# Kernel optimization log

Hardware: AMD Instinct MI355X
Metric: run time of the kernel (lower is better)

The kernel has to match this reference:

```python
import jax, jax.numpy as jnp
import numpy as np

C = 256; G = 16; GC = C // G; K = 3; P = K * K
N = 4; H = 64; W = 64
PAD = 1; OFFSET_SCALE = 1.0; LN_EPS = 1e-5


def setup_inputs() -> dict:
    key = jax.random.key(0)
    ks = jax.random.split(key, 8)
    s = 0.02
    return {
        "x": jax.random.normal(ks[0], (N, C, H, W), jnp.float32),
        "dw_w": jax.random.normal(ks[1], (C, 1, K, K), jnp.float32) * s,
        "dw_b": jnp.zeros((C,), jnp.float32),
        "ln_g": jnp.ones((C,), jnp.float32),
        "ln_b": jnp.zeros((C,), jnp.float32),
        "off_w": jax.random.normal(ks[2], (C, G * P * 2), jnp.float32) * s,
        "off_b": jnp.zeros((G * P * 2,), jnp.float32),
        "mask_w": jax.random.normal(ks[3], (C, G * P), jnp.float32) * s,
        "mask_b": jnp.zeros((G * P,), jnp.float32),
        "inp_w": jax.random.normal(ks[4], (C, C), jnp.float32) * s,
        "inp_b": jnp.zeros((C,), jnp.float32),
        "out_w": jax.random.normal(ks[5], (C, C), jnp.float32) * s,
        "out_b": jnp.zeros((C,), jnp.float32),
    }


def _dcnv3_nchw(x, dw_w, dw_b, ln_g, ln_b, off_w, off_b, mask_w, mask_b,
                inp_w, inp_b, out_w, out_b):
    # NCHW -> NHWC (wrapper permute)
    xn = jnp.transpose(x, (0, 2, 3, 1))                      # (N,H,W,C)
    x_proj = xn @ inp_w + inp_b                              # input_proj

    # offset/mask branch: depthwise conv (NCHW) -> LayerNorm (channels-last) -> GELU
    x1 = jax.lax.conv_general_dilated(
        x, dw_w, window_strides=(1, 1), padding=((PAD, PAD), (PAD, PAD)),
        dimension_numbers=("NCHW", "OIHW", "NCHW"), feature_group_count=C)
    x1 = jnp.transpose(x1, (0, 2, 3, 1)) + dw_b
    mu = x1.mean(-1, keepdims=True)
    var = ((x1 - mu) ** 2).mean(-1, keepdims=True)
    x1 = (x1 - mu) * jax.lax.rsqrt(var + LN_EPS) * ln_g + ln_b
    x1 = jax.nn.gelu(x1, approximate=False)

    offset = (x1 @ off_w + off_b).reshape(N, H, W, G, P, 2)  # (x,y) pairs
    mask = jax.nn.softmax((x1 @ mask_w + mask_b).reshape(N, H, W, G, P), axis=-1)

    # pad sampled feature map with zeros (F.pad before sampling)
    xp = jnp.pad(x_proj, ((0, 0), (PAD, PAD), (PAD, PAD), (0, 0)))
    Hin, Win = H + 2 * PAD, W + 2 * PAD
    xg = xp.reshape(N, Hin, Win, G, GC)

    # reference points, normalized by padded size
    ref_y = (jnp.arange(H, dtype=jnp.float32) + PAD + 0.5) / Hin
    ref_x = (jnp.arange(W, dtype=jnp.float32) + PAD + 0.5) / Win
    ref = jnp.stack([jnp.broadcast_to(ref_x[None, :], (H, W)),
                     jnp.broadcast_to(ref_y[:, None], (H, W))], -1)  # (H,W,2)

    # dilation grid: x varies in the outer loop (torch meshgrid 'ij')
    d = jnp.arange(K, dtype=jnp.float32) - (K - 1) // 2     # [-1,0,1]
    gx = jnp.repeat(d, K) / Win
    gy = jnp.tile(d, K) / Hin
    grid = jnp.stack([gx, gy], -1)                           # (P,2)

    norm = jnp.array([Win, Hin], jnp.float32)
    loc = (ref[None, :, :, None, None, :] + grid * OFFSET_SCALE
           + offset * OFFSET_SCALE / norm)                   # (N,H,W,G,P,2)

    # grid_sample bilinear, align_corners=False, zero padding
    px = loc[..., 0] * Win - 0.5
    py = loc[..., 1] * Hin - 0.5
    x0 = jnp.floor(px); y0 = jnp.floor(py)
    wx = px - x0; wy = py - y0
    x0i = x0.astype(jnp.int32); y0i = y0.astype(jnp.int32)

    n_idx = jnp.arange(N)[:, None, None, None, None]
    g_idx = jnp.arange(G)[None, None, None, :, None]

    def corner(iy, ix, w):
        valid = (iy >= 0) & (iy < Hin) & (ix >= 0) & (ix < Win)
        v = xg[n_idx, jnp.clip(iy, 0, Hin - 1), jnp.clip(ix, 0, Win - 1), g_idx]
        wgt = jnp.where(valid, w, 0.0) * mask                # fold mask into weights
        return jnp.einsum("nhwgp,nhwgpc->nhwgc", wgt, v)

    out = (corner(y0i, x0i, (1 - wy) * (1 - wx))
           + corner(y0i, x0i + 1, (1 - wy) * wx)
           + corner(y0i + 1, x0i, wy * (1 - wx))
           + corner(y0i + 1, x0i + 1, wy * wx))               # (N,H,W,G,GC)

    out = out.reshape(N, H, W, C) @ out_w + out_b            # output_proj
    return jnp.transpose(out, (0, 3, 1, 2))                  # NHWC -> NCHW


def reference(x, dw_w, dw_b, ln_g, ln_b, off_w, off_b, mask_w, mask_b,
              inp_w, inp_b, out_w, out_b):
    return _dcnv3_nchw(x, dw_w, dw_b, ln_g, ln_b, off_w, off_b,
                       mask_w, mask_b, inp_w, inp_b, out_w, out_b)
```

## Files before the change

### kernel.cpp

```cpp
#include <hip/hip_runtime.h>
#include <hip/hip_bf16.h>
#include <math.h>


using bf16x8 = __attribute__((ext_vector_type(8))) short;
using f32x4  = __attribute__((ext_vector_type(4))) float;

#define GLOBAL_AS __attribute__((address_space(1)))
#define LDS_AS    __attribute__((address_space(3)))

static __device__ inline void g2lds16(const void* g, void* l) {
  __builtin_amdgcn_global_load_lds((const GLOBAL_AS int*)g, (LDS_AS int*)l, 16, 0, 0);
}
static __device__ inline unsigned short f2bf(float v) {
  __hip_bfloat16 b = __float2bfloat16(v);
  return *reinterpret_cast<unsigned short*>(&b);
}
static __device__ inline float us2f(unsigned short u) {
  union { unsigned u; float f; } c; c.u = ((unsigned)u) << 16; return c.f;
}

__global__ __launch_bounds__(256) void prep_xt_k(
    const float* __restrict__ x,
    const float* __restrict__ inp_w, const float* __restrict__ off_w,
    const float* __restrict__ off_b, const float* __restrict__ mask_w,
    const float* __restrict__ mask_b, const float* __restrict__ out_w,
    __hip_bfloat16* __restrict__ BtI, __hip_bfloat16* __restrict__ BtOM,
    __hip_bfloat16* __restrict__ BtO, float* __restrict__ bOM,
    __hip_bfloat16* __restrict__ xT)
{
  __shared__ float tile[32][65];
  const int b = blockIdx.x, t = threadIdx.x;
  if (b < 1024) {
    if (b < 256) {
      int n = b;
      BtI[n * 256 + t] = __float2bfloat16(inp_w[t * 256 + n]);
    } else if (b < 768) {
      int n = b - 256;
      float v = 0.f;
      if (n < 288) v = off_w[t * 288 + n];
      else if (n < 432) v = mask_w[t * 144 + (n - 288)];
      BtOM[n * 256 + t] = __float2bfloat16(v);
      if (b == 256) {
        for (int idx = t; idx < 512; idx += 256) {
          float bv = (idx < 288) ? off_b[idx] : ((idx < 432) ? mask_b[idx - 288] : 0.f);
          bOM[idx] = bv;
        }
      }
    } else {
      int n = b - 768;
      BtO[n * 256 + t] = __float2bfloat16(out_w[t * 256 + n]);
    }
    return;
  }
  const int i = b - 1024;
  const int hw0 = (i & 63) * 64, c0 = ((i >> 6) & 7) * 32, n4 = i >> 9;
  #pragma unroll
  for (int r = 0; r < 8; ++r) {
    int idx = t + r * 256;
    int cl = idx >> 6, wl = idx & 63;
    tile[cl][wl] = x[(size_t)n4 * 1048576 + (size_t)(c0 + cl) * 4096 + hw0 + wl];
  }
  __syncthreads();
  #pragma unroll
  for (int r = 0; r < 2; ++r) {
    int idx = t + r * 256;
    int pixl = idx >> 3, cq = idx & 7;
    unsigned short b0 = f2bf(tile[cq * 4 + 0][pixl]);
    unsigned short b1 = f2bf(tile[cq * 4 + 1][pixl]);
    unsigned short b2 = f2bf(tile[cq * 4 + 2][pixl]);
    unsigned short b3 = f2bf(tile[cq * 4 + 3][pixl]);
    uint2 u;
    u.x = (unsigned)b0 | ((unsigned)b1 << 16);
    u.y = (unsigned)b2 | ((unsigned)b3 << 16);
    *(uint2*)&xT[((size_t)n4 * 4096 + hw0 + pixl) * 256 + c0 + cq * 4] = u;
  }
}

struct G64 {
  f32x4 acc[2][2];
  int lane, quad, lr, wm, wn;
};

static __device__ inline void g64_loop(
    G64& g, const __hip_bfloat16* __restrict__ A,
    const __hip_bfloat16* __restrict__ Bt, size_t m0, int n0,
    short* As, short* Bs, int t)
{
  #pragma unroll
  for (int i = 0; i < 2; ++i)
    #pragma unroll
    for (int j = 0; j < 2; ++j)
      g.acc[i][j] = (f32x4){0.f, 0.f, 0.f, 0.f};
  const int row = t >> 2, kq = t & 3;
  for (int kt = 0; kt < 256; kt += 32) {
    g2lds16(A + (m0 + row) * 256 + kt + kq * 8, (char*)As + t * 16);
    g2lds16(Bt + (size_t)(n0 + row) * 256 + kt + kq * 8, (char*)Bs + t * 16);
    __syncthreads();
    bf16x8 bfv[2];
    #pragma unroll
    for (int ni = 0; ni < 2; ++ni)
      bfv[ni] = *(const bf16x8*)&Bs[(g.wn * 32 + ni * 16 + g.lr) * 32 + g.quad * 8];
    #pragma unroll
    for (int mi = 0; mi < 2; ++mi) {
      bf16x8 af = *(const bf16x8*)&As[(g.wm * 32 + mi * 16 + g.lr) * 32 + g.quad * 8];
      #pragma unroll
      for (int ni = 0; ni < 2; ++ni)
        g.acc[mi][ni] = __builtin_amdgcn_mfma_f32_16x16x32_bf16(af, bfv[ni], g.acc[mi][ni], 0, 0, 0);
    }
    __syncthreads();
  }
}

__global__ __launch_bounds__(1024) void stage2_gi_k(
    const __hip_bfloat16* __restrict__ xT,
    const float* __restrict__ dw_w, const float* __restrict__ dw_b,
    const float* __restrict__ ln_g, const float* __restrict__ ln_b,
    const __hip_bfloat16* __restrict__ BtOM, const float* __restrict__ bOM,
    __hip_bfloat16* __restrict__ om,
    const __hip_bfloat16* __restrict__ BtI, const float* __restrict__ inp_b,
    __hip_bfloat16* __restrict__ xpu)
{
  __shared__ __align__(16) char smem[62464];
  const int bid = blockIdx.x;

  if (bid >= 256) {
    const int sb = threadIdx.x >> 8;
    const int t = threadIdx.x & 255;
    const int tile = (bid - 256) * 4 + sb;
    const int n0 = (tile & 3) * 64;
    const size_t m0 = (size_t)(tile >> 2) * 64;
    short* As = (short*)(smem + sb * 8192);
    short* Bs = (short*)(smem + sb * 8192 + 4096);

    G64 g;
    g.lane = t & 63; g.quad = g.lane >> 4; g.lr = g.lane & 15;
    int wave = t >> 6;
    g.wm = wave >> 1; g.wn = wave & 1;
    g64_loop(g, xT, BtI, m0, n0, As, Bs, t);

    #pragma unroll
    for (int mi = 0; mi < 2; ++mi) {
      #pragma unroll
      for (int ni = 0; ni < 2; ++ni) {
        int col = n0 + g.wn * 32 + ni * 16 + g.lr;
        float bv = inp_b[col];
        #pragma unroll
        for (int reg = 0; reg < 4; ++reg) {
          size_t m = m0 + g.wm * 32 + mi * 16 + g.quad * 4 + reg;
          xpu[m * 256 + col] = __float2bfloat16(g.acc[mi][ni][reg] + bv);
        }
      }
    }
    return;
  }

  unsigned short* x1t = (unsigned short*)smem;
  unsigned short* xs  = (unsigned short*)(smem + 33792);
  float* wgt  = (float*)(smem + 33792 + 15360);
  float* psq  = (float*)(smem + 33792 + 15360 + 1152);
  float* murs = (float*)(smem + 33792 + 15360 + 1152 + 8192);
  short* Bs   = (short*)(smem + 33792);

  const int blk = ((bid & 7) << 5) | (bid >> 3);
  const int n4 = blk >> 6, h = blk & 63;
  const int t = threadIdx.x;
  const int w = t & 63, q = t >> 6;

  float s1 = 0.f, s2 = 0.f;
  for (int chunk = 0; chunk < 8; ++chunk) {
    const int ch0 = chunk * 32;
    if (t < 768) {
      int r = t >> 8, i = t & 255;
      int px = i >> 2, cq = i & 3;
      int hh = h + r - 1;
      uint4 v = {0, 0, 0, 0};
      if ((unsigned)hh < 64u)
        v = *(const uint4*)(xT + ((size_t)n4 * 4096 + (size_t)hh * 64 + px) * 256 + ch0 + cq * 8);
      *(uint4*)&xs[(r * 64 + px) * 40 + cq * 8] = v;
    }
    if (t < 288) {
      int p = t >> 5, lc = t & 31;
      wgt[p * 32 + lc] = dw_w[(ch0 + lc) * 9 + p];
    }
    __syncthreads();
    {
      int c = ch0 + 2 * q;
      float a0 = dw_b[c], a1 = dw_b[c + 1];
      #pragma unroll
      for (int p = 0; p < 9; ++p) {
        int dh = p / 3, dwd = p % 3 - 1;
        int ww = w + dwd;
        if ((unsigned)ww < 64u) {
          unsigned xv = *(const unsigned*)&xs[(dh * 64 + ww) * 40 + 2 * q];
          float wa = wgt[p * 32 + 2 * q], wb = wgt[p * 32 + 2 * q + 1];
          a0 = fmaf(us2f((unsigned short)(xv & 0xffff)), wa, a0);
          a1 = fmaf(us2f((unsigned short)(xv >> 16)), wb, a1);
        }
      }
      s1 += a0 + a1;
      s2 = fmaf(a0, a0, fmaf(a1, a1, s2));
      unsigned pk = (unsigned)f2bf(a0) | ((unsigned)f2bf(a1) << 16);
      *(unsigned*)&x1t[w * 264 + c] = pk;
    }
    __syncthreads();
  }

  psq[q * 64 + w] = s1;
  psq[1024 + q * 64 + w] = s2;
  __syncthreads();
  if (t < 64) {
    float a = 0.f, b = 0.f;
    #pragma unroll
    for (int j = 0; j < 16; ++j) { a += psq[j * 64 + t]; b += psq[1024 + j * 64 + t]; }
    float mu = a * (1.f / 256.f);
    murs[t] = mu;
    murs[64 + t] = rsqrtf(b * (1.f / 256.f) - mu * mu + 1e-5f);
  }
  __syncthreads();
  {
    float mu = murs[w], rs = murs[64 + w];
    #pragma unroll
    for (int chunk = 0; chunk < 8; ++chunk) {
      int c = chunk * 32 + 2 * q;
      unsigned pk = *(const unsigned*)&x1t[w * 264 + c];
      float v0 = us2f((unsigned short)(pk & 0xffff));
      float v1 = us2f((unsigned short)(pk >> 16));
      float y0 = fmaf((v0 - mu) * rs, ln_g[c], ln_b[c]);
      float y1 = fmaf((v1 - mu) * rs, ln_g[c + 1], ln_b[c + 1]);
      float g0 = 0.5f * y0 * (1.f + erff(y0 * 0.70710678f));
      float g1 = 0.5f * y1 * (1.f + erff(y1 * 0.70710678f));
      *(unsigned*)&x1t[w * 264 + c] = (unsigned)f2bf(g0) | ((unsigned)f2bf(g1) << 16);
    }
  }
  __syncthreads();

  const int wave = t >> 6, lane = t & 63;
  const int quad = lane >> 4, lr = lane & 15;
  const int wm = wave >> 2, wn = wave & 3;
  f32x4 acc[7];
  #pragma unroll
  for (int i = 0; i < 7; ++i) acc[i] = (f32x4){0.f, 0.f, 0.f, 0.f};

  for (int kt = 0; kt < 256; kt += 32) {
    __syncthreads();
    {
      int col = t >> 2, kq = t & 3;
      g2lds16(BtOM + (size_t)col * 256 + kt + kq * 8, (char*)Bs + t * 16);
      int j = t + 1024;
      if (j < 1792) {
        col = j >> 2; kq = j & 3;
        g2lds16(BtOM + (size_t)col * 256 + kt + kq * 8, (char*)Bs + j * 16);
      }
    }
    __syncthreads();
    bf16x8 af = *(const bf16x8*)&x1t[(wm * 16 + lr) * 264 + kt + quad * 8];
    #pragma unroll
    for (int ni = 0; ni < 7; ++ni) {
      bf16x8 bf = *(const bf16x8*)&Bs[(wn * 112 + ni * 16 + lr) * 32 + quad * 8];
      acc[ni] = __builtin_amdgcn_mfma_f32_16x16x32_bf16(af, bf, acc[ni], 0, 0, 0);
    }
  }

  const size_t pix0 = (size_t)n4 * 4096 + (size_t)h * 64;
  #pragma unroll
  for (int ni = 0; ni < 7; ++ni) {
    int col = wn * 112 + ni * 16 + lr;
    if (col < 432) {
      float bv = bOM[col];
      #pragma unroll
      for (int reg = 0; reg < 4; ++reg) {
        int m = wm * 16 + quad * 4 + reg;
        om[(pix0 + m) * 448 + col] = __float2bfloat16(acc[ni][reg] + bv);
      }
    }
  }
}

__global__ __launch_bounds__(1024) void fused_so_k(
    const __hip_bfloat16* __restrict__ xpu, const __hip_bfloat16* __restrict__ om,
    const __hip_bfloat16* __restrict__ BtO, const float* __restrict__ out_b,
    float* __restrict__ out)
{
  __shared__ __align__(16) char smem[50176];
  unsigned short* st = (unsigned short*)smem;
  short* Bs = (short*)(smem + 33792);

  const int bid = blockIdx.x;
  const int swz = ((bid & 7) << 5) | (bid >> 3);
  const int pix0 = swz << 6;
  const int t = threadIdx.x;

  {
    const int pl = t >> 4, g = t & 15;
    const int pix = pix0 + pl;
    const int n4s = pix >> 12;
    const int hw = pix & 4095;
    const int h = hw >> 6, w = hw & 63;
    const unsigned short* omp = (const unsigned short*)om + (size_t)pix * 448;

    float mk[9];
    {
      float mx = -1e30f;
      #pragma unroll
      for (int p = 0; p < 9; ++p) { mk[p] = us2f(omp[288 + g * 9 + p]); mx = fmaxf(mx, mk[p]); }
      float se = 0.f;
      #pragma unroll
      for (int p = 0; p < 9; ++p) { mk[p] = __expf(mk[p] - mx); se += mk[p]; }
      float inv = 1.f / se;
      #pragma unroll
      for (int p = 0; p < 9; ++p) mk[p] *= inv;
    }

    const __hip_bfloat16* xpg = xpu + (g << 4);
    float ax[16];
    #pragma unroll
    for (int i = 0; i < 16; ++i) ax[i] = 0.f;

    auto corner = [&](int iy, int ix, float wt) {
      if ((unsigned)(iy - 1) >= 64u || (unsigned)(ix - 1) >= 64u) return;
      const __hip_bfloat16* src =
          xpg + ((size_t)((n4s << 12) + (iy - 1) * 64 + (ix - 1)) << 8);
      uint4 u0 = *(const uint4*)src;
      uint4 u1 = *(const uint4*)(src + 8);
      const unsigned uu[8] = {u0.x, u0.y, u0.z, u0.w, u1.x, u1.y, u1.z, u1.w};
      #pragma unroll
      for (int i = 0; i < 8; ++i) {
        float lo = us2f((unsigned short)(uu[i] & 0xffff));
        float hi = us2f((unsigned short)(uu[i] >> 16));
        ax[2 * i + 0] = fmaf(wt, lo, ax[2 * i + 0]);
        ax[2 * i + 1] = fmaf(wt, hi, ax[2 * i + 1]);
      }
    };

    #pragma unroll
    for (int p = 0; p < 9; ++p) {
      float ox = us2f(omp[g * 18 + 2 * p]), oy = us2f(omp[g * 18 + 2 * p + 1]);
      float px = (float)(w + p / 3) + ox;
      float py = (float)(h + p % 3) + oy;
      float xf = floorf(px), yf = floorf(py);
      float wx = px - xf, wy = py - yf;
      int ix = (int)xf, iy = (int)yf;
      float m = mk[p];
      corner(iy,     ix,     (1.f - wy) * (1.f - wx) * m);
      corner(iy,     ix + 1, (1.f - wy) * wx * m);
      corner(iy + 1, ix,     wy * (1.f - wx) * m);
      corner(iy + 1, ix + 1, wy * wx * m);
    }

    unsigned short ub[16];
    #pragma unroll
    for (int i = 0; i < 16; ++i) ub[i] = f2bf(ax[i]);
    uint4 u0, u1;
    u0.x = (unsigned)ub[0] | ((unsigned)ub[1] << 16);
    u0.y = (unsigned)ub[2] | ((unsigned)ub[3] << 16);
    u0.z = (unsigned)ub[4] | ((unsigned)ub[5] << 16);
    u0.w = (unsigned)ub[6] | ((unsigned)ub[7] << 16);
    u1.x = (unsigned)ub[8] | ((unsigned)ub[9] << 16);
    u1.y = (unsigned)ub[10] | ((unsigned)ub[11] << 16);
    u1.z = (unsigned)ub[12] | ((unsigned)ub[13] << 16);
    u1.w = (unsigned)ub[14] | ((unsigned)ub[15] << 16);
    *(uint4*)&st[pl * 264 + g * 16] = u0;
    *(uint4*)&st[pl * 264 + g * 16 + 8] = u1;
  }

  const int wave = t >> 6, lane = t & 63;
  const int quad = lane >> 4, lr = lane & 15;
  const int wm = wave >> 2, wn = wave & 3;
  f32x4 acc[4];
  #pragma unroll
  for (int i = 0; i < 4; ++i) acc[i] = (f32x4){0.f, 0.f, 0.f, 0.f};

  for (int kt = 0; kt < 256; kt += 32) {
    __syncthreads();
    {
      int col = t >> 2, kq = t & 3;
      g2lds16(BtO + (size_t)col * 256 + kt + kq * 8, (char*)Bs + t * 16);
    }
    __syncthreads();
    bf16x8 af = *(const bf16x8*)&st[(wm * 16 + lr) * 264 + kt + quad * 8];
    #pragma unroll
    for (int ni = 0; ni < 4; ++ni) {
      bf16x8 bf = *(const bf16x8*)&Bs[(wn * 64 + ni * 16 + lr) * 32 + quad * 8];
      acc[ni] = __builtin_amdgcn_mfma_f32_16x16x32_bf16(af, bf, acc[ni], 0, 0, 0);
    }
  }

  const int n4 = pix0 >> 12, hw0 = pix0 & 4095;
  #pragma unroll
  for (int ni = 0; ni < 4; ++ni) {
    int col = wn * 64 + ni * 16 + lr;
    float bv = out_b[col];
    float4 v;
    v.x = acc[ni][0] + bv; v.y = acc[ni][1] + bv;
    v.z = acc[ni][2] + bv; v.w = acc[ni][3] + bv;
    *(float4*)&out[(size_t)(n4 * 256 + col) * 4096 + hw0 + wm * 16 + quad * 4] = v;
  }
}

extern "C" void kernel_launch(void* const* d_in, const int* in_sizes, int n_in,
                              void* d_out, int out_size, void* d_ws, size_t ws_size,
                              hipStream_t stream) {
  const float* x      = (const float*)d_in[0];
  const float* dw_w   = (const float*)d_in[1];
  const float* dw_b   = (const float*)d_in[2];
  const float* ln_g   = (const float*)d_in[3];
  const float* ln_b   = (const float*)d_in[4];
  const float* off_w  = (const float*)d_in[5];
  const float* off_b  = (const float*)d_in[6];
  const float* mask_w = (const float*)d_in[7];
  const float* mask_b = (const float*)d_in[8];
  const float* inp_w  = (const float*)d_in[9];
  const float* inp_b  = (const float*)d_in[10];
  const float* out_w  = (const float*)d_in[11];
  const float* out_b  = (const float*)d_in[12];
  float* out = (float*)d_out;

  char* w0 = (char*)d_ws;
  __hip_bfloat16* xpu  = (__hip_bfloat16*)(w0);
  __hip_bfloat16* xT   = (__hip_bfloat16*)(w0 + 8388608);
  __hip_bfloat16* om   = (__hip_bfloat16*)(w0 + 16777216);
  __hip_bfloat16* BtI  = (__hip_bfloat16*)(w0 + 31457280);
  __hip_bfloat16* BtOM = (__hip_bfloat16*)(w0 + 31588352);
  __hip_bfloat16* BtO  = (__hip_bfloat16*)(w0 + 31850496);
  float*          bOM  = (float*)(w0 + 31981568);
  if (ws_size < 31983616) return;

  prep_xt_k<<<3072, 256, 0, stream>>>(x, inp_w, off_w, off_b, mask_w, mask_b,
                                      out_w, BtI, BtOM, BtO, bOM, xT);
  stage2_gi_k<<<512, 1024, 0, stream>>>(xT, dw_w, dw_b, ln_g, ln_b, BtOM, bOM, om,
                                        BtI, inp_b, xpu);
  fused_so_k<<<256, 1024, 0, stream>>>(xpu, om, BtO, out_b, out);
}
```

Before: 161.4 us.

## Load GEMM operands directly from global, process depthwise conv in halves, shrink sampling blocks

The three GEMM loops no longer stage B (and A for the input projection) through LDS with per-step barriers. Each wave now loads its bf16x8 fragments straight from global memory into registers, relying on cache reuse. The depthwise conv now runs over two 128-channel halves with fewer barriers, and keeps its fp32 results in registers instead of round-tripping them through bf16 LDS. The sampling/output kernel moves to 512 blocks of 512 threads with 32 pixels each, which removes the LDS weight staging but costs more redundant global reads of the weights.

```diff
diff --git a/kernel.cpp b/kernel.cpp
--- a/kernel.cpp
+++ b/kernel.cpp
@@ -6,12 +6,6 @@
 using bf16x8 = __attribute__((ext_vector_type(8))) short;
 using f32x4  = __attribute__((ext_vector_type(4))) float;
 
-#define GLOBAL_AS __attribute__((address_space(1)))
-#define LDS_AS    __attribute__((address_space(3)))
-
-static __device__ inline void g2lds16(const void* g, void* l) {
-  __builtin_amdgcn_global_load_lds((const GLOBAL_AS int*)g, (LDS_AS int*)l, 16, 0, 0);
-}
 static __device__ inline unsigned short f2bf(float v) {
   __hip_bfloat16 b = __float2bfloat16(v);
   return *reinterpret_cast<unsigned short*>(&b);
@@ -77,41 +71,6 @@
   }
 }
 
-struct G64 {
-  f32x4 acc[2][2];
-  int lane, quad, lr, wm, wn;
-};
-
-static __device__ inline void g64_loop(
-    G64& g, const __hip_bfloat16* __restrict__ A,
-    const __hip_bfloat16* __restrict__ Bt, size_t m0, int n0,
-    short* As, short* Bs, int t)
-{
-  #pragma unroll
-  for (int i = 0; i < 2; ++i)
-    #pragma unroll
-    for (int j = 0; j < 2; ++j)
-      g.acc[i][j] = (f32x4){0.f, 0.f, 0.f, 0.f};
-  const int row = t >> 2, kq = t & 3;
-  for (int kt = 0; kt < 256; kt += 32) {
-    g2lds16(A + (m0 + row) * 256 + kt + kq * 8, (char*)As + t * 16);
-    g2lds16(Bt + (size_t)(n0 + row) * 256 + kt + kq * 8, (char*)Bs + t * 16);
-    __syncthreads();
-    bf16x8 bfv[2];
-    #pragma unroll
-    for (int ni = 0; ni < 2; ++ni)
-      bfv[ni] = *(const bf16x8*)&Bs[(g.wn * 32 + ni * 16 + g.lr) * 32 + g.quad * 8];
-    #pragma unroll
-    for (int mi = 0; mi < 2; ++mi) {
-      bf16x8 af = *(const bf16x8*)&As[(g.wm * 32 + mi * 16 + g.lr) * 32 + g.quad * 8];
-      #pragma unroll
-      for (int ni = 0; ni < 2; ++ni)
-        g.acc[mi][ni] = __builtin_amdgcn_mfma_f32_16x16x32_bf16(af, bfv[ni], g.acc[mi][ni], 0, 0, 0);
-    }
-    __syncthreads();
-  }
-}
-
 __global__ __launch_bounds__(1024) void stage2_gi_k(
     const __hip_bfloat16* __restrict__ xT,
     const float* __restrict__ dw_w, const float* __restrict__ dw_b,
@@ -121,7 +80,7 @@
     const __hip_bfloat16* __restrict__ BtI, const float* __restrict__ inp_b,
     __hip_bfloat16* __restrict__ xpu)
 {
-  __shared__ __align__(16) char smem[62464];
+  __shared__ __align__(16) char smem[65024];
   const int bid = blockIdx.x;
 
   if (bid >= 256) {
@@ -130,25 +89,39 @@
     const int tile = (bid - 256) * 4 + sb;
     const int n0 = (tile & 3) * 64;
     const size_t m0 = (size_t)(tile >> 2) * 64;
-    short* As = (short*)(smem + sb * 8192);
-    short* Bs = (short*)(smem + sb * 8192 + 4096);
-
-    G64 g;
-    g.lane = t & 63; g.quad = g.lane >> 4; g.lr = g.lane & 15;
-    int wave = t >> 6;
-    g.wm = wave >> 1; g.wn = wave & 1;
-    g64_loop(g, xT, BtI, m0, n0, As, Bs, t);
-
+    const int lane = t & 63, quad = lane >> 4, lr = lane & 15;
+    const int wave = t >> 6, wm = wave >> 1, wn = wave & 1;
+
+    f32x4 acc[2][2];
+    #pragma unroll
+    for (int i = 0; i < 2; ++i)
+      #pragma unroll
+      for (int j = 0; j < 2; ++j)
+        acc[i][j] = (f32x4){0.f, 0.f, 0.f, 0.f};
+
+    const __hip_bfloat16* ap = xT + (m0 + wm * 32 + lr) * 256 + quad * 8;
+    const __hip_bfloat16* bp = BtI + (size_t)(n0 + wn * 32 + lr) * 256 + quad * 8;
+    #pragma unroll 2
+    for (int kt = 0; kt < 256; kt += 32) {
+      bf16x8 a0 = *(const bf16x8*)(ap + kt);
+      bf16x8 a1 = *(const bf16x8*)(ap + 4096 + kt);
+      bf16x8 b0 = *(const bf16x8*)(bp + kt);
+      bf16x8 b1 = *(const bf16x8*)(bp + 4096 + kt);
+      acc[0][0] = __builtin_amdgcn_mfma_f32_16x16x32_bf16(a0, b0, acc[0][0], 0, 0, 0);
+      acc[0][1] = __builtin_amdgcn_mfma_f32_16x16x32_bf16(a0, b1, acc[0][1], 0, 0, 0);
+      acc[1][0] = __builtin_amdgcn_mfma_f32_16x16x32_bf16(a1, b0, acc[1][0], 0, 0, 0);
+      acc[1][1] = __builtin_amdgcn_mfma_f32_16x16x32_bf16(a1, b1, acc[1][1], 0, 0, 0);
+    }
     #pragma unroll
     for (int mi = 0; mi < 2; ++mi) {
       #pragma unroll
       for (int ni = 0; ni < 2; ++ni) {
-        int col = n0 + g.wn * 32 + ni * 16 + g.lr;
+        int col = n0 + wn * 32 + ni * 16 + lr;
         float bv = inp_b[col];
         #pragma unroll
         for (int reg = 0; reg < 4; ++reg) {
-          size_t m = m0 + g.wm * 32 + mi * 16 + g.quad * 4 + reg;
-          xpu[m * 256 + col] = __float2bfloat16(g.acc[mi][ni][reg] + bv);
+          size_t m = m0 + wm * 32 + mi * 16 + quad * 4 + reg;
+          xpu[m * 256 + col] = __float2bfloat16(acc[mi][ni][reg] + bv);
         }
       }
     }
@@ -156,54 +129,60 @@
   }
 
   unsigned short* x1t = (unsigned short*)smem;
-  unsigned short* xs  = (unsigned short*)(smem + 33792);
-  float* wgt  = (float*)(smem + 33792 + 15360);
-  float* psq  = (float*)(smem + 33792 + 15360 + 1152);
-  float* murs = (float*)(smem + 33792 + 15360 + 1152 + 8192);
-  short* Bs   = (short*)(smem + 33792);
+  unsigned short* xs  = (unsigned short*)smem;
+  float* psq  = (float*)(smem + 52224);
+  float* wgt  = (float*)(smem + 60416);
+  float* murs = (float*)(smem + 60416);
 
   const int blk = ((bid & 7) << 5) | (bid >> 3);
   const int n4 = blk >> 6, h = blk & 63;
   const int t = threadIdx.x;
   const int w = t & 63, q = t >> 6;
 
+  float av[16];
   float s1 = 0.f, s2 = 0.f;
-  for (int chunk = 0; chunk < 8; ++chunk) {
-    const int ch0 = chunk * 32;
-    if (t < 768) {
-      int r = t >> 8, i = t & 255;
-      int px = i >> 2, cq = i & 3;
+
+  #pragma unroll
+  for (int half = 0; half < 2; ++half) {
+    const int ch0 = half * 128;
+    if (half) __syncthreads();
+    #pragma unroll
+    for (int it = 0; it < 3; ++it) {
+      int i = t + it * 1024;
+      int rp = i >> 4, cq = i & 15;
+      int r = rp >> 6, px = rp & 63;
       int hh = h + r - 1;
       uint4 v = {0, 0, 0, 0};
       if ((unsigned)hh < 64u)
         v = *(const uint4*)(xT + ((size_t)n4 * 4096 + (size_t)hh * 64 + px) * 256 + ch0 + cq * 8);
-      *(uint4*)&xs[(r * 64 + px) * 40 + cq * 8] = v;
-    }
-    if (t < 288) {
-      int p = t >> 5, lc = t & 31;
-      wgt[p * 32 + lc] = dw_w[(ch0 + lc) * 9 + p];
+      *(uint4*)&xs[rp * 136 + cq * 8] = v;
+    }
+    for (int idx = t; idx < 1152; idx += 1024) {
+      int p = idx >> 7, lc = idx & 127;
+      wgt[p * 128 + lc] = dw_w[(ch0 + lc) * 9 + p];
     }
     __syncthreads();
-    {
-      int c = ch0 + 2 * q;
+    #pragma unroll
+    for (int ck = 0; ck < 4; ++ck) {
+      int cl = ck * 32 + 2 * q;
+      int c = ch0 + cl;
       float a0 = dw_b[c], a1 = dw_b[c + 1];
       #pragma unroll
       for (int p = 0; p < 9; ++p) {
         int dh = p / 3, dwd = p % 3 - 1;
         int ww = w + dwd;
         if ((unsigned)ww < 64u) {
-          unsigned xv = *(const unsigned*)&xs[(dh * 64 + ww) * 40 + 2 * q];
-          float wa = wgt[p * 32 + 2 * q], wb = wgt[p * 32 + 2 * q + 1];
+          unsigned xv = *(const unsigned*)&xs[(dh * 64 + ww) * 136 + cl];
+          float wa = wgt[p * 128 + cl], wb = wgt[p * 128 + cl + 1];
           a0 = fmaf(us2f((unsigned short)(xv & 0xffff)), wa, a0);
           a1 = fmaf(us2f((unsigned short)(xv >> 16)), wb, a1);
         }
       }
       s1 += a0 + a1;
       s2 = fmaf(a0, a0, fmaf(a1, a1, s2));
-      unsigned pk = (unsigned)f2bf(a0) | ((unsigned)f2bf(a1) << 16);
-      *(unsigned*)&x1t[w * 264 + c] = pk;
-    }
-    __syncthreads();
+      av[(half * 4 + ck) * 2] = a0;
+      av[(half * 4 + ck) * 2 + 1] = a1;
+    }
   }
 
   psq[q * 64 + w] = s1;
@@ -221,13 +200,10 @@
   {
     float mu = murs[w], rs = murs[64 + w];
     #pragma unroll
-    for (int chunk = 0; chunk < 8; ++chunk) {
-      int c = chunk * 32 + 2 * q;
-      unsigned pk = *(const unsigned*)&x1t[w * 264 + c];
-      float v0 = us2f((unsigned short)(pk & 0xffff));
-      float v1 = us2f((unsigned short)(pk >> 16));
-      float y0 = fmaf((v0 - mu) * rs, ln_g[c], ln_b[c]);
-      float y1 = fmaf((v1 - mu) * rs, ln_g[c + 1], ln_b[c + 1]);
+    for (int ck = 0; ck < 8; ++ck) {
+      int c = ck * 32 + 2 * q;
+      float y0 = fmaf((av[ck * 2] - mu) * rs, ln_g[c], ln_b[c]);
+      float y1 = fmaf((av[ck * 2 + 1] - mu) * rs, ln_g[c + 1], ln_b[c + 1]);
       float g0 = 0.5f * y0 * (1.f + erff(y0 * 0.70710678f));
       float g1 = 0.5f * y1 * (1.f + erff(y1 * 0.70710678f));
       *(unsigned*)&x1t[w * 264 + c] = (unsigned)f2bf(g0) | ((unsigned)f2bf(g1) << 16);
@@ -242,24 +218,18 @@
   #pragma unroll
   for (int i = 0; i < 7; ++i) acc[i] = (f32x4){0.f, 0.f, 0.f, 0.f};
 
+  const __hip_bfloat16* bp = BtOM + (size_t)(wn * 112 + lr) * 256 + quad * 8;
+  const unsigned short* abase = &x1t[(wm * 16 + lr) * 264 + quad * 8];
+  #pragma unroll 2
   for (int kt = 0; kt < 256; kt += 32) {
-    __syncthreads();
-    {
-      int col = t >> 2, kq = t & 3;
-      g2lds16(BtOM + (size_t)col * 256 + kt + kq * 8, (char*)Bs + t * 16);
-      int j = t + 1024;
-      if (j < 1792) {
-        col = j >> 2; kq = j & 3;
-        g2lds16(BtOM + (size_t)col * 256 + kt + kq * 8, (char*)Bs + j * 16);
-      }
-    }
-    __syncthreads();
-    bf16x8 af = *(const bf16x8*)&x1t[(wm * 16 + lr) * 264 + kt + quad * 8];
-    #pragma unroll
-    for (int ni = 0; ni < 7; ++ni) {
-      bf16x8 bf = *(const bf16x8*)&Bs[(wn * 112 + ni * 16 + lr) * 32 + quad * 8];
-      acc[ni] = __builtin_amdgcn_mfma_f32_16x16x32_bf16(af, bf, acc[ni], 0, 0, 0);
-    }
+    bf16x8 af = *(const bf16x8*)(abase + kt);
+    bf16x8 bfr[7];
+    #pragma unroll
+    for (int ni = 0; ni < 7; ++ni)
+      bfr[ni] = *(const bf16x8*)(bp + (size_t)ni * 4096 + kt);
+    #pragma unroll
+    for (int ni = 0; ni < 7; ++ni)
+      acc[ni] = __builtin_amdgcn_mfma_f32_16x16x32_bf16(af, bfr[ni], acc[ni], 0, 0, 0);
   }
 
   const size_t pix0 = (size_t)n4 * 4096 + (size_t)h * 64;
@@ -277,18 +247,16 @@
   }
 }
 
-__global__ __launch_bounds__(1024) void fused_so_k(
+__global__ __launch_bounds__(512) void fused_so_k(
     const __hip_bfloat16* __restrict__ xpu, const __hip_bfloat16* __restrict__ om,
     const __hip_bfloat16* __restrict__ BtO, const float* __restrict__ out_b,
     float* __restrict__ out)
 {
-  __shared__ __align__(16) char smem[50176];
-  unsigned short* st = (unsigned short*)smem;
-  short* Bs = (short*)(smem + 33792);
+  __shared__ __align__(16) unsigned short st[32 * 264];
 
   const int bid = blockIdx.x;
-  const int swz = ((bid & 7) << 5) | (bid >> 3);
-  const int pix0 = swz << 6;
+  const int swz = ((bid & 7) << 6) | (bid >> 3);
+  const int pix0 = swz << 5;
   const int t = threadIdx.x;
 
   {
@@ -363,6 +331,7 @@
     *(uint4*)&st[pl * 264 + g * 16] = u0;
     *(uint4*)&st[pl * 264 + g * 16 + 8] = u1;
   }
+  __syncthreads();
 
   const int wave = t >> 6, lane = t & 63;
   const int quad = lane >> 4, lr = lane & 15;
@@ -371,17 +340,14 @@
   #pragma unroll
   for (int i = 0; i < 4; ++i) acc[i] = (f32x4){0.f, 0.f, 0.f, 0.f};
 
+  const __hip_bfloat16* bp = BtO + (size_t)(wn * 64 + lr) * 256 + quad * 8;
+  const unsigned short* abase = &st[(wm * 16 + lr) * 264 + quad * 8];
+  #pragma unroll 2
   for (int kt = 0; kt < 256; kt += 32) {
-    __syncthreads();
-    {
-      int col = t >> 2, kq = t & 3;
-      g2lds16(BtO + (size_t)col * 256 + kt + kq * 8, (char*)Bs + t * 16);
-    }
-    __syncthreads();
-    bf16x8 af = *(const bf16x8*)&st[(wm * 16 + lr) * 264 + kt + quad * 8];
+    bf16x8 af = *(const bf16x8*)(abase + kt);
     #pragma unroll
     for (int ni = 0; ni < 4; ++ni) {
-      bf16x8 bf = *(const bf16x8*)&Bs[(wn * 64 + ni * 16 + lr) * 32 + quad * 8];
+      bf16x8 bf = *(const bf16x8*)(bp + (size_t)ni * 4096 + kt);
       acc[ni] = __builtin_amdgcn_mfma_f32_16x16x32_bf16(af, bf, acc[ni], 0, 0, 0);
     }
   }
@@ -430,5 +396,5 @@
                                       out_w, BtI, BtOM, BtO, bOM, xT);
   stage2_gi_k<<<512, 1024, 0, stream>>>(xT, dw_w, dw_b, ln_g, ln_b, BtOM, bOM, om,
                                         BtI, inp_b, xpu);
-  fused_so_k<<<256, 1024, 0, stream>>>(xpu, om, BtO, out_b, out);
-}
+  fused_so_k<<<512, 512, 0, stream>>>(xpu, om, BtO, out_b, out);
+}
```

Measured after the change: 190.5 us. 1.18x slower.

## Compute depthwise conv directly from NCHW fp32 input with wave shuffles and register-held results

Applied to the files above, without the earlier changes.

The depthwise 3x3 conv in the offset/mask branch now reads the original fp32 NCHW input directly instead of staging bf16 transposed rows through LDS. Horizontal neighbours come from wave shuffles, and the per-channel results stay in registers for the LayerNorm/GELU pass, so the bf16 round-trip through LDS is gone. This removes eight LDS staging rounds and their barriers, and uses fp32 inputs rather than bf16. The cost is more register pressure (16 extra floats) and uncached strided global reads of x across three rows.

```diff
diff --git a/kernel.cpp b/kernel.cpp
--- a/kernel.cpp
+++ b/kernel.cpp
@@ -113,6 +113,7 @@
 }
 
 __global__ __launch_bounds__(1024) void stage2_gi_k(
+    const float* __restrict__ x,
     const __hip_bfloat16* __restrict__ xT,
     const float* __restrict__ dw_w, const float* __restrict__ dw_b,
     const float* __restrict__ ln_g, const float* __restrict__ ln_b,
@@ -156,10 +157,8 @@
   }
 
   unsigned short* x1t = (unsigned short*)smem;
-  unsigned short* xs  = (unsigned short*)(smem + 33792);
-  float* wgt  = (float*)(smem + 33792 + 15360);
-  float* psq  = (float*)(smem + 33792 + 15360 + 1152);
-  float* murs = (float*)(smem + 33792 + 15360 + 1152 + 8192);
+  float* psq  = (float*)(smem + 33792);
+  float* murs = (float*)(smem + 41984);
   short* Bs   = (short*)(smem + 33792);
 
   const int blk = ((bid & 7) << 5) | (bid >> 3);
@@ -167,43 +166,38 @@
   const int t = threadIdx.x;
   const int w = t & 63, q = t >> 6;
 
+  const float* xb = x + (size_t)n4 * 1048576;
+  const bool hm = (h > 0), hp = (h < 63);
+  float av[16];
   float s1 = 0.f, s2 = 0.f;
-  for (int chunk = 0; chunk < 8; ++chunk) {
-    const int ch0 = chunk * 32;
-    if (t < 768) {
-      int r = t >> 8, i = t & 255;
-      int px = i >> 2, cq = i & 3;
-      int hh = h + r - 1;
-      uint4 v = {0, 0, 0, 0};
-      if ((unsigned)hh < 64u)
-        v = *(const uint4*)(xT + ((size_t)n4 * 4096 + (size_t)hh * 64 + px) * 256 + ch0 + cq * 8);
-      *(uint4*)&xs[(r * 64 + px) * 40 + cq * 8] = v;
-    }
-    if (t < 288) {
-      int p = t >> 5, lc = t & 31;
-      wgt[p * 32 + lc] = dw_w[(ch0 + lc) * 9 + p];
-    }
-    __syncthreads();
-    {
-      int c = ch0 + 2 * q;
-      float a0 = dw_b[c], a1 = dw_b[c + 1];
-      #pragma unroll
-      for (int p = 0; p < 9; ++p) {
-        int dh = p / 3, dwd = p % 3 - 1;
-        int ww = w + dwd;
-        if ((unsigned)ww < 64u) {
-          unsigned xv = *(const unsigned*)&xs[(dh * 64 + ww) * 40 + 2 * q];
-          float wa = wgt[p * 32 + 2 * q], wb = wgt[p * 32 + 2 * q + 1];
-          a0 = fmaf(us2f((unsigned short)(xv & 0xffff)), wa, a0);
-          a1 = fmaf(us2f((unsigned short)(xv >> 16)), wb, a1);
-        }
-      }
-      s1 += a0 + a1;
-      s2 = fmaf(a0, a0, fmaf(a1, a1, s2));
-      unsigned pk = (unsigned)f2bf(a0) | ((unsigned)f2bf(a1) << 16);
-      *(unsigned*)&x1t[w * 264 + c] = pk;
-    }
-    __syncthreads();
+
+  #pragma unroll 2
+  for (int j = 0; j < 8; ++j) {
+    #pragma unroll
+    for (int u = 0; u < 2; ++u) {
+      const int c = q * 16 + 2 * j + u;
+      const float* xc = xb + (size_t)c * 4096 + h * 64 + w;
+      float v0 = hm ? xc[-64] : 0.f;
+      float v1 = xc[0];
+      float v2 = hp ? xc[64] : 0.f;
+      const float* wp = dw_w + c * 9;
+      float a = dw_b[c];
+      float vr0 = v0, vr1 = v1, vr2 = v2;
+      #pragma unroll
+      for (int dh = 0; dh < 3; ++dh) {
+        float v = (dh == 0) ? vr0 : (dh == 1) ? vr1 : vr2;
+        float vm = __shfl(v, w - 1, 64);
+        float vp = __shfl(v, w + 1, 64);
+        if (w == 0)  vm = 0.f;
+        if (w == 63) vp = 0.f;
+        a = fmaf(vm, wp[dh * 3 + 0], a);
+        a = fmaf(v,  wp[dh * 3 + 1], a);
+        a = fmaf(vp, wp[dh * 3 + 2], a);
+      }
+      s1 += a;
+      s2 = fmaf(a, a, s2);
+      av[2 * j + u] = a;
+    }
   }
 
   psq[q * 64 + w] = s1;
@@ -221,13 +215,10 @@
   {
     float mu = murs[w], rs = murs[64 + w];
     #pragma unroll
-    for (int chunk = 0; chunk < 8; ++chunk) {
-      int c = chunk * 32 + 2 * q;
-      unsigned pk = *(const unsigned*)&x1t[w * 264 + c];
-      float v0 = us2f((unsigned short)(pk & 0xffff));
-      float v1 = us2f((unsigned short)(pk >> 16));
-      float y0 = fmaf((v0 - mu) * rs, ln_g[c], ln_b[c]);
-      float y1 = fmaf((v1 - mu) * rs, ln_g[c + 1], ln_b[c + 1]);
+    for (int j = 0; j < 8; ++j) {
+      int c = q * 16 + 2 * j;
+      float y0 = fmaf((av[2 * j] - mu) * rs, ln_g[c], ln_b[c]);
+      float y1 = fmaf((av[2 * j + 1] - mu) * rs, ln_g[c + 1], ln_b[c + 1]);
       float g0 = 0.5f * y0 * (1.f + erff(y0 * 0.70710678f));
       float g1 = 0.5f * y1 * (1.f + erff(y1 * 0.70710678f));
       *(unsigned*)&x1t[w * 264 + c] = (unsigned)f2bf(g0) | ((unsigned)f2bf(g1) << 16);
@@ -247,10 +238,10 @@
     {
       int col = t >> 2, kq = t & 3;
       g2lds16(BtOM + (size_t)col * 256 + kt + kq * 8, (char*)Bs + t * 16);
-      int j = t + 1024;
-      if (j < 1792) {
-        col = j >> 2; kq = j & 3;
-        g2lds16(BtOM + (size_t)col * 256 + kt + kq * 8, (char*)Bs + j * 16);
+      int jj = t + 1024;
+      if (jj < 1792) {
+        col = jj >> 2; kq = jj & 3;
+        g2lds16(BtOM + (size_t)col * 256 + kt + kq * 8, (char*)Bs + jj * 16);
       }
     }
     __syncthreads();
@@ -428,7 +419,7 @@
 
   prep_xt_k<<<3072, 256, 0, stream>>>(x, inp_w, off_w, off_b, mask_w, mask_b,
                                       out_w, BtI, BtOM, BtO, bOM, xT);
-  stage2_gi_k<<<512, 1024, 0, stream>>>(xT, dw_w, dw_b, ln_g, ln_b, BtOM, bOM, om,
-                                        BtI, inp_b, xpu);
+  stage2_gi_k<<<512, 1024, 0, stream>>>(x, xT, dw_w, dw_b, ln_g, ln_b, BtOM, bOM,
+                                        om, BtI, inp_b, xpu);
   fused_so_k<<<256, 1024, 0, stream>>>(xpu, om, BtO, out_b, out);
 }
```

New measurement: 157.6 us. 1.02x faster.
